# Kernel optimization log

Hardware: AMD Instinct MI355X
Metric: run time of the kernel (lower is better)

The kernel has to match this reference:

```python
import jax, jax.numpy as jnp
import numpy as np
from math import factorial

LMAX = 2
C_DIM = 128
N = 50000
# (l1, l2, l_out) 'uuu' (channel-wise, no weights) instructions, as in the module ([:3])
INSTR = [(2, 2, 0), (1, 2, 1), (1, 1, 2)]


def _f(n):
    return float(factorial(int(n)))


def _su2_cg(j1, m1, j2, m2, j3, m3):
    # Clebsch-Gordan <j1 m1 j2 m2 | j3 m3> (Racah formula), complex SU(2) basis
    if m3 != m1 + m2:
        return 0.0
    vmin = int(max(-j1 + j2 + m3, -j1 + m1, 0))
    vmax = int(min(j2 + j3 + m1, j3 - j1 + j2, j3 + m3))
    pref = ((2 * j3 + 1) * _f(j3 + j1 - j2) * _f(j3 - j1 + j2) * _f(j1 + j2 - j3) / _f(j1 + j2 + j3 + 1)
            * _f(j3 + m3) * _f(j3 - m3) / (_f(j1 - m1) * _f(j1 + m1) * _f(j2 - m2) * _f(j2 + m2))) ** 0.5
    s = 0.0
    for v in range(vmin, vmax + 1):
        s += (-1.0) ** (v + j2 + m2) / _f(v) * _f(j2 + j3 + m1 - v) * _f(j1 - m1 + v) / (
            _f(j3 - j1 + j2 - v) * _f(j3 + m3 - v) * _f(v + j1 - j2 - m3))
    return pref * s


def _q_real_to_complex(l):
    # e3nn change-of-basis from real to complex spherical harmonics
    q = np.zeros((2 * l + 1, 2 * l + 1), dtype=np.complex128)
    for m in range(-l, 0):
        q[l + m, l + abs(m)] = 1.0 / np.sqrt(2)
        q[l + m, l - abs(m)] = -1j / np.sqrt(2)
    q[l, l] = 1.0
    for m in range(1, l + 1):
        q[l + m, l + abs(m)] = (-1) ** m / np.sqrt(2)
        q[l + m, l - abs(m)] = 1j * (-1) ** m / np.sqrt(2)
    return (-1j) ** l * q


def wigner_3j(l1, l2, l3):
    # real-basis Wigner 3j, unit Frobenius norm (e3nn convention)
    Csu2 = np.zeros((2 * l1 + 1, 2 * l2 + 1, 2 * l3 + 1), dtype=np.complex128)
    for i, m1 in enumerate(range(-l1, l1 + 1)):
        for k, m2 in enumerate(range(-l2, l2 + 1)):
            for n, m3 in enumerate(range(-l3, l3 + 1)):
                Csu2[i, k, n] = _su2_cg(l1, m1, l2, m2, l3, m3)
    Q1, Q2, Q3 = _q_real_to_complex(l1), _q_real_to_complex(l2), _q_real_to_complex(l3)
    C = np.einsum('ij,kl,mn,ikn->jlm', Q1, Q2, np.conj(Q3.T), Csu2)
    assert np.abs(C.imag).max() < 1e-7
    C = C.real
    return (C / np.linalg.norm(C)).astype(np.float32)


W3J = {(l1, l2, lo): jnp.asarray(wigner_3j(l1, l2, lo)) for (l1, l2, lo) in INSTR}


def so3_linear(x, W, b):
    # per-degree block-diagonal linear; x: [N, (LMAX+1)^2, Cin], W: [LMAX+1, Cout, Cin], b: [Cout] (l=0 only)
    outs = []
    for l in range(LMAX + 1):
        y = jnp.einsum('nmc,dc->nmd', x[:, l * l:(l + 1) * (l + 1), :], W[l])
        if l == 0:
            y = y + b
        outs.append(y)
    return jnp.concatenate(outs, axis=1)


def tensor_product_uuu(x1, x2):
    # sparse CG tensor product, channel-shared ('uuu'), no path weights
    out = jnp.zeros_like(x1)
    for (l1, l2, lo) in INSTR:
        w3j = W3J[(l1, l2, lo)]
        alpha = float((2 * lo + 1) ** 0.5)  # component normalization
        blk = alpha * jnp.einsum('ijk,nic,njc->nkc', w3j,
                                 x1[:, l1 * l1:(l1 + 1) ** 2, :],
                                 x2[:, l2 * l2:(l2 + 1) ** 2, :])
        out = out.at[:, lo * lo:(lo + 1) ** 2, :].add(blk)
    return out


def setup_inputs() -> dict:
    key = jax.random.key(0)
    ks = jax.random.split(key, 7)
    scale = 1.0 / np.sqrt(C_DIM)
    m_dim = (LMAX + 1) ** 2  # 9
    return {
        'irreps_x': jax.random.normal(ks[0], (N, m_dim, C_DIM), jnp.float32),
        'W_left': jax.random.normal(ks[1], (LMAX + 1, C_DIM, C_DIM), jnp.float32) * scale,
        'b_left': jax.random.normal(ks[2], (C_DIM,), jnp.float32) * scale,
        'W_right': jax.random.normal(ks[3], (LMAX + 1, C_DIM, C_DIM), jnp.float32) * scale,
        'b_right': jax.random.normal(ks[4], (C_DIM,), jnp.float32) * scale,
        'W_final': jax.random.normal(ks[5], (LMAX + 1, C_DIM, C_DIM), jnp.float32) * scale,
        'b_final': jax.random.normal(ks[6], (C_DIM,), jnp.float32) * scale,
    }


def reference(irreps_x, W_left, b_left, W_right, b_right, W_final, b_final):
    xl = so3_linear(irreps_x, W_left, b_left)
    xr = so3_linear(irreps_x, W_right, b_right)
    out = tensor_product_uuu(xl, xr)
    return so3_linear(out, W_final, b_final)  # [N, 9, C]
```

## Files before the change

kernel.cpp:

```cpp
#include <hip/hip_runtime.h>
#include <cmath>
#include <complex>

typedef unsigned short u16;
typedef unsigned int u32;
typedef __bf16 bf16x8 __attribute__((ext_vector_type(8)));
typedef __bf16 bf16x2 __attribute__((ext_vector_type(2)));
typedef float f32x4 __attribute__((ext_vector_type(4)));
typedef float f32x2 __attribute__((ext_vector_type(2)));

#define CD 128
#define TILE_N 8
#define XS 136
#define LS 132

#define SMEM_TOTAL (72 * XS + 64 * LS + 64 * LS)

struct TPW { float w220[25]; float w121[45]; float w112[45]; };

__device__ __forceinline__ u32 pk2(float a, float b) {
  bf16x2 h;
  h.x = (__bf16)a;
  h.y = (__bf16)b;
  return __builtin_bit_cast(u32, h);
}
__device__ __forceinline__ f32x2 unpk(u32 v) {
  f32x2 r;
  r.x = __uint_as_float(v << 16);
  r.y = __uint_as_float(v & 0xffff0000u);
  return r;
}

__global__ void cvt_weights_kernel(const float* __restrict__ Wl,
                                   const float* __restrict__ Wr,
                                   const float* __restrict__ Wf,
                                   u16* __restrict__ ws) {
  int idx = (blockIdx.x * 256 + threadIdx.x) * 8;
  const float* src; int off;
  if (idx < 49152)      { src = Wl; off = idx; }
  else if (idx < 98304) { src = Wr; off = idx - 49152; }
  else                  { src = Wf; off = idx - 98304; }
  float4 a = *(const float4*)(src + off);
  float4 b = *(const float4*)(src + off + 4);
  uint4 v;
  v.x = pk2(a.x, a.y);
  v.y = pk2(a.z, a.w);
  v.z = pk2(b.x, b.y);
  v.w = pk2(b.z, b.w);
  *(uint4*)(ws + idx) = v;
}

__global__ __launch_bounds__(256, 3)
void fused_kernel(const float* __restrict__ x, const u16* __restrict__ ws,
                  const float* __restrict__ bfin, float* __restrict__ out,
                  int N, TPW tw) {
  __shared__ __align__(16) u16 smem[SMEM_TOTAL];
  u16* bufX = smem;
  u16* sTP  = smem;
  u16* sL   = smem + 72 * XS;
  u16* sR   = smem + 72 * XS + 64 * LS;

  const int tid  = threadIdx.x;
  const int n0   = blockIdx.x * TILE_N;
  const int w    = tid >> 6;
  const int lane = tid & 63;
  const int q    = lane >> 4;
  const int lr   = lane & 15;

  const int mat = w >> 1;
  const int wl  = w & 1;
  u16* dstA = mat ? sR : sL;
  const u16* wsA = ws + mat * 3 * 16384;

  uint4 bfa[2][2][4];
#pragma unroll
  for (int ci = 0; ci < 2; ++ci) {
    int dcol = (wl * 4 + ci) * 16 + lr;
#pragma unroll
    for (int kk = 0; kk < 4; ++kk) {
      bfa[ci][0][kk] = *(const uint4*)(wsA + 16384     + dcol * CD + kk * 32 + q * 8);
      bfa[ci][1][kk] = *(const uint4*)(wsA + 2 * 16384 + dcol * CD + kk * 32 + q * 8);
    }
  }
  const int dc0 = w * 16 + lr;
  const int dc1 = dc0 + 64;
  float bias0 = bfin[dc0];
  float bias1 = bfin[dc1];

#pragma unroll
  for (int it = 0; it < 4; ++it) {
    int e = (it * 256 + tid) * 8;
    int r = e >> 7;
    int c = e & 127;
    int n = n0 + (r & 7);
    if (n >= N) n = N - 1;
    int grow = (n * 9 + 1 + (r >> 3)) * CD + c;
    float4 a = *(const float4*)(x + grow);
    float4 b = *(const float4*)(x + grow + 4);
    uint4 v;
    v.x = pk2(a.x, a.y);
    v.y = pk2(a.z, a.w);
    v.z = pk2(b.x, b.y);
    v.w = pk2(b.z, b.w);
    *(uint4*)(bufX + r * XS + c) = v;
  }
  __syncthreads();

#pragma unroll
  for (int p = 0; p < 2; ++p) {
    if (p == 1) {
#pragma unroll
      for (int ci = 0; ci < 2; ++ci) {
        int dcol = (wl * 4 + 2 + ci) * 16 + lr;
#pragma unroll
        for (int kk = 0; kk < 4; ++kk) {
          bfa[ci][0][kk] = *(const uint4*)(wsA + 16384     + dcol * CD + kk * 32 + q * 8);
          bfa[ci][1][kk] = *(const uint4*)(wsA + 2 * 16384 + dcol * CD + kk * 32 + q * 8);
        }
      }
    }
#pragma unroll
    for (int rt = 0; rt < 5; ++rt) {
      const int l2f   = (rt >= 2) ? 1 : 0;
      const int rows  = l2f ? 40 : 24;
      const int gbase = l2f ? (rt - 2) * 16 : rt * 16;
      const int boff  = l2f ? 24 : 0;
      int ga = gbase + lr; if (ga > rows - 1) ga = rows - 1;
      const int arow = boff + ga;
      uint4 av[4];
#pragma unroll
      for (int kk = 0; kk < 4; ++kk)
        av[kk] = *(const uint4*)(bufX + arow * XS + kk * 32 + q * 8);
#pragma unroll
      for (int ci = 0; ci < 2; ++ci) {
        int dcol = (wl * 4 + 2 * p + ci) * 16 + lr;
        f32x4 acc = {0.f, 0.f, 0.f, 0.f};
#pragma unroll
        for (int kk = 0; kk < 4; ++kk) {
          acc = __builtin_amdgcn_mfma_f32_16x16x32_bf16(
              __builtin_bit_cast(bf16x8, av[kk]),
              __builtin_bit_cast(bf16x8, bfa[ci][l2f][kk]),
              acc, 0, 0, 0);
        }
        int g0 = gbase + q * 4;
        if (g0 < rows) {
          u32 p01 = pk2(acc[0], acc[1]);
          u32 p23 = pk2(acc[2], acc[3]);
          u16* d = dstA + (boff + g0) * LS + dcol;
          d[0]      = (u16)p01;
          d[LS]     = (u16)(p01 >> 16);
          d[2 * LS] = (u16)p23;
          d[3 * LS] = (u16)(p23 >> 16);
        }
      }
    }
  }
  __syncthreads();

#pragma unroll
  for (int iter = 0; iter < 2; ++iter) {
    int id = iter * 256 + tid;
    int cb = (id & 63) * 2;
    int n  = id >> 6;
    const u16* pL = sL + n * LS + cb;
    const u16* pR = sR + n * LS + cb;
    f32x2 xl1[3], xr1[3], xl2[5], xr2[5];
#pragma unroll
    for (int i = 0; i < 3; ++i) {
      xl1[i] = unpk(*(const u32*)(pL + i * 8 * LS));
      xr1[i] = unpk(*(const u32*)(pR + i * 8 * LS));
    }
#pragma unroll
    for (int j = 0; j < 5; ++j) {
      xl2[j] = unpk(*(const u32*)(pL + (24 + j * 8) * LS));
      xr2[j] = unpk(*(const u32*)(pR + (24 + j * 8) * LS));
    }
    f32x2 o0 = {0.f, 0.f};
#pragma unroll
    for (int i = 0; i < 5; ++i) {
      f32x2 t = {0.f, 0.f};
#pragma unroll
      for (int j = 0; j < 5; ++j) t += tw.w220[i * 5 + j] * xr2[j];
      o0 += xl2[i] * t;
    }
    f32x2 o1[3] = {{0.f,0.f},{0.f,0.f},{0.f,0.f}};
#pragma unroll
    for (int i = 0; i < 3; ++i)
#pragma unroll
      for (int j = 0; j < 5; ++j) {
        f32x2 pr = xl1[i] * xr2[j];
#pragma unroll
        for (int k = 0; k < 3; ++k) o1[k] += tw.w121[(i * 5 + j) * 3 + k] * pr;
      }
    f32x2 o2[5] = {{0.f,0.f},{0.f,0.f},{0.f,0.f},{0.f,0.f},{0.f,0.f}};
#pragma unroll
    for (int i = 0; i < 3; ++i)
#pragma unroll
      for (int j = 0; j < 3; ++j) {
        f32x2 pr = xl1[i] * xr1[j];
#pragma unroll
        for (int k = 0; k < 5; ++k) o2[k] += tw.w112[(i * 3 + j) * 5 + k] * pr;
      }
    u16* pT = sTP + n * XS + cb;
    *(u32*)(pT) = pk2(o0.x, o0.y);
#pragma unroll
    for (int k = 0; k < 3; ++k) *(u32*)(pT + (1 + k) * 8 * XS) = pk2(o1[k].x, o1[k].y);
#pragma unroll
    for (int k = 0; k < 5; ++k) *(u32*)(pT + (4 + k) * 8 * XS) = pk2(o2[k].x, o2[k].y);
  }

  const u16* wsf = ws + 6 * 16384;
  uint4 bc0[4], bc1[4];
#pragma unroll
  for (int kk = 0; kk < 4; ++kk) {
    bc0[kk] = *(const uint4*)(wsf + dc0 * CD + kk * 32 + q * 8);
    bc1[kk] = *(const uint4*)(wsf + dc1 * CD + kk * 32 + q * 8);
  }
  __syncthreads();

#pragma unroll
  for (int l = 0; l < 3; ++l) {
    if (l > 0) {
#pragma unroll
      for (int kk = 0; kk < 4; ++kk) {
        bc0[kk] = *(const uint4*)(wsf + l * 16384 + dc0 * CD + kk * 32 + q * 8);
        bc1[kk] = *(const uint4*)(wsf + l * 16384 + dc1 * CD + kk * 32 + q * 8);
      }
    }
    const int rows   = (l == 0) ? 8 : (l == 1 ? 24 : 40);
    const int soff   = (l == 0) ? 0 : (l == 1 ? 8 : 32);
    const int ntiles = (l == 0) ? 1 : (l == 1 ? 2 : 3);
#pragma unroll
    for (int t = 0; t < 3; ++t) {
      if (t >= ntiles) continue;
      int ga = t * 16 + lr; if (ga > rows - 1) ga = rows - 1;
      const int arow = soff + ga;
      uint4 av[4];
#pragma unroll
      for (int kk = 0; kk < 4; ++kk)
        av[kk] = *(const uint4*)(sTP + arow * XS + kk * 32 + q * 8);
      f32x4 a0 = {0.f, 0.f, 0.f, 0.f};
      f32x4 a1 = {0.f, 0.f, 0.f, 0.f};
#pragma unroll
      for (int kk = 0; kk < 4; ++kk) {
        a0 = __builtin_amdgcn_mfma_f32_16x16x32_bf16(
            __builtin_bit_cast(bf16x8, av[kk]),
            __builtin_bit_cast(bf16x8, bc0[kk]), a0, 0, 0, 0);
        a1 = __builtin_amdgcn_mfma_f32_16x16x32_bf16(
            __builtin_bit_cast(bf16x8, av[kk]),
            __builtin_bit_cast(bf16x8, bc1[kk]), a1, 0, 0, 0);
      }
#pragma unroll
      for (int reg = 0; reg < 4; ++reg) {
        int gg = t * 16 + q * 4 + reg;
        if (gg < rows) {
          int m = l * l + (gg >> 3);
          int n = n0 + (gg & 7);
          if (n < N) {
            float v0 = a0[reg], v1 = a1[reg];
            if (l == 0) { v0 += bias0; v1 += bias1; }
            out[(n * 9 + m) * CD + dc0] = v0;
            out[(n * 9 + m) * CD + dc1] = v1;
          }
        }
      }
    }
  }
}

typedef std::complex<double> cd;

static double factd(int n) { double r = 1.0; for (int i = 2; i <= n; ++i) r *= i; return r; }

static double su2_cg(int j1, int m1, int j2, int m2, int j3, int m3) {
  if (m3 != m1 + m2) return 0.0;
  int vmin = -j1 + j2 + m3; if (-j1 + m1 > vmin) vmin = -j1 + m1; if (0 > vmin) vmin = 0;
  int vmax = j2 + j3 + m1; if (j3 - j1 + j2 < vmax) vmax = j3 - j1 + j2; if (j3 + m3 < vmax) vmax = j3 + m3;
  double pref = std::sqrt((2.0 * j3 + 1.0) * factd(j3 + j1 - j2) * factd(j3 - j1 + j2)
                          * factd(j1 + j2 - j3) / factd(j1 + j2 + j3 + 1)
                          * factd(j3 + m3) * factd(j3 - m3)
                          / (factd(j1 - m1) * factd(j1 + m1) * factd(j2 - m2) * factd(j2 + m2)));
  double s = 0.0;
  for (int v = vmin; v <= vmax; ++v) {
    double sgn = ((v + j2 + m2) & 1) ? -1.0 : 1.0;
    s += sgn / factd(v) * factd(j2 + j3 + m1 - v) * factd(j1 - m1 + v)
         / (factd(j3 - j1 + j2 - v) * factd(j3 + m3 - v) * factd(v + j1 - j2 - m3));
  }
  return pref * s;
}

static void qmat(int l, cd q[5][5]) {
  for (int a = 0; a < 5; ++a) for (int b = 0; b < 5; ++b) q[a][b] = 0.0;
  const double is2 = 1.0 / std::sqrt(2.0);
  for (int m = -l; m < 0; ++m) {
    q[l + m][l - m] = is2;
    q[l + m][l + m] = cd(0.0, -is2);
  }
  q[l][l] = 1.0;
  for (int m = 1; m <= l; ++m) {
    double s = (m & 1) ? -1.0 : 1.0;
    q[l + m][l + m] = s * is2;
    q[l + m][l - m] = cd(0.0, s * is2);
  }
  cd f(1.0, 0.0);
  for (int i = 0; i < l; ++i) f *= cd(0.0, -1.0);
  for (int a = 0; a < 5; ++a) for (int b = 0; b < 5; ++b) q[a][b] *= f;
}

static void wigner3j(int l1, int l2, int l3, double* C) {
  int d1 = 2 * l1 + 1, d2 = 2 * l2 + 1, d3 = 2 * l3 + 1;
  cd Q1[5][5], Q2[5][5], Q3[5][5];
  qmat(l1, Q1); qmat(l2, Q2); qmat(l3, Q3);
  cd Csu2[5][5][5];
  for (int i = 0; i < d1; ++i)
    for (int k = 0; k < d2; ++k)
      for (int n = 0; n < d3; ++n)
        Csu2[i][k][n] = su2_cg(l1, i - l1, l2, k - l2, l3, n - l3);
  double norm = 0.0;
  for (int j = 0; j < d1; ++j)
    for (int lx = 0; lx < d2; ++lx)
      for (int m = 0; m < d3; ++m) {
        cd acc(0.0, 0.0);
        for (int i = 0; i < d1; ++i)
          for (int k = 0; k < d2; ++k)
            for (int n = 0; n < d3; ++n)
              acc += Q1[i][j] * Q2[k][lx] * std::conj(Q3[n][m]) * Csu2[i][k][n];
        C[(j * d2 + lx) * d3 + m] = acc.real();
        norm += acc.real() * acc.real();
      }
  norm = std::sqrt(norm);
  for (int t = 0; t < d1 * d2 * d3; ++t) C[t] /= norm;
}

extern "C" void kernel_launch(void* const* d_in, const int* in_sizes, int n_in,
                              void* d_out, int out_size, void* d_ws, size_t ws_size,
                              hipStream_t stream) {
  const float* x    = (const float*)d_in[0];
  const float* Wl   = (const float*)d_in[1];
  const float* Wr   = (const float*)d_in[3];
  const float* Wf   = (const float*)d_in[5];
  const float* bfin = (const float*)d_in[6];
  float* out = (float*)d_out;
  const int N = in_sizes[0] / (9 * CD);

  TPW tw;
  double c220[25], c121[45], c112[45];
  wigner3j(2, 2, 0, c220);
  wigner3j(1, 2, 1, c121);
  wigner3j(1, 1, 2, c112);
  const double a1 = std::sqrt(3.0), a2 = std::sqrt(5.0);
  for (int i = 0; i < 25; ++i) tw.w220[i] = (float)c220[i];
  for (int i = 0; i < 45; ++i) tw.w121[i] = (float)(a1 * c121[i]);
  for (int i = 0; i < 45; ++i) tw.w112[i] = (float)(a2 * c112[i]);

  u16* ws = (u16*)d_ws;
  cvt_weights_kernel<<<72, 256, 0, stream>>>(Wl, Wr, Wf, ws);
  int grid = (N + TILE_N - 1) / TILE_N;
  fused_kernel<<<grid, 256, 0, stream>>>(x, ws, bfin, out, N, tw);
}
```

Baseline: 489.5 us.

## Convert fused kernel to persistent grid-stride loop over node tiles

Launches a fixed grid of 768 blocks that loop over the 8-node tiles instead of one block per tile. The weight fragment loads are restructured so that each pass processes the l=1 and l=2 row tiles with two column blocks held in registers, reloading B fragments per phase. The intent is to cut block launch and scheduling overhead and to reuse per-block setup such as the bias loads. In exchange, weights are now reloaded every tile and there is an extra barrier per iteration, and the grid may be too small to hide latency.

```diff
diff --git a/kernel.cpp b/kernel.cpp
--- a/kernel.cpp
+++ b/kernel.cpp
@@ -13,6 +13,7 @@
 #define TILE_N 8
 #define XS 136
 #define LS 132
+#define GRID_BLOCKS 768
 
 #define SMEM_TOTAL (72 * XS + 64 * LS + 64 * LS)
 
@@ -29,6 +30,26 @@
   r.x = __uint_as_float(v << 16);
   r.y = __uint_as_float(v & 0xffff0000u);
   return r;
+}
+
+__device__ __forceinline__ void ldw4(uint4* dst, const u16* base) {
+#pragma unroll
+  for (int kk = 0; kk < 4; ++kk)
+    dst[kk] = *(const uint4*)(base + kk * 32);
+}
+
+__device__ __forceinline__ f32x4 mf(const uint4& a, const uint4& b, f32x4 c) {
+  return __builtin_amdgcn_mfma_f32_16x16x32_bf16(
+      __builtin_bit_cast(bf16x8, a), __builtin_bit_cast(bf16x8, b), c, 0, 0, 0);
+}
+
+__device__ __forceinline__ void stA(u16* d, const f32x4& a) {
+  u32 p01 = pk2(a[0], a[1]);
+  u32 p23 = pk2(a[2], a[3]);
+  d[0]      = (u16)p01;
+  d[LS]     = (u16)(p01 >> 16);
+  d[2 * LS] = (u16)p23;
+  d[3 * LS] = (u16)(p23 >> 16);
 }
 
 __global__ void cvt_weights_kernel(const float* __restrict__ Wl,
@@ -61,7 +82,6 @@
   u16* sR   = smem + 72 * XS + 64 * LS;
 
   const int tid  = threadIdx.x;
-  const int n0   = blockIdx.x * TILE_N;
   const int w    = tid >> 6;
   const int lane = tid & 63;
   const int q    = lane >> 4;
@@ -71,196 +91,188 @@
   const int wl  = w & 1;
   u16* dstA = mat ? sR : sL;
   const u16* wsA = ws + mat * 3 * 16384;
-
-  uint4 bfa[2][2][4];
-#pragma unroll
-  for (int ci = 0; ci < 2; ++ci) {
-    int dcol = (wl * 4 + ci) * 16 + lr;
-#pragma unroll
-    for (int kk = 0; kk < 4; ++kk) {
-      bfa[ci][0][kk] = *(const uint4*)(wsA + 16384     + dcol * CD + kk * 32 + q * 8);
-      bfa[ci][1][kk] = *(const uint4*)(wsA + 2 * 16384 + dcol * CD + kk * 32 + q * 8);
-    }
-  }
+  const u16* wsf = ws + 6 * 16384;
+
   const int dc0 = w * 16 + lr;
   const int dc1 = dc0 + 64;
-  float bias0 = bfin[dc0];
-  float bias1 = bfin[dc1];
-
-#pragma unroll
-  for (int it = 0; it < 4; ++it) {
-    int e = (it * 256 + tid) * 8;
-    int r = e >> 7;
-    int c = e & 127;
-    int n = n0 + (r & 7);
-    if (n >= N) n = N - 1;
-    int grow = (n * 9 + 1 + (r >> 3)) * CD + c;
-    float4 a = *(const float4*)(x + grow);
-    float4 b = *(const float4*)(x + grow + 4);
-    uint4 v;
-    v.x = pk2(a.x, a.y);
-    v.y = pk2(a.z, a.w);
-    v.z = pk2(b.x, b.y);
-    v.w = pk2(b.z, b.w);
-    *(uint4*)(bufX + r * XS + c) = v;
-  }
-  __syncthreads();
-
-#pragma unroll
-  for (int p = 0; p < 2; ++p) {
-    if (p == 1) {
-#pragma unroll
-      for (int ci = 0; ci < 2; ++ci) {
-        int dcol = (wl * 4 + 2 + ci) * 16 + lr;
+  const float bias0 = bfin[dc0];
+  const float bias1 = bfin[dc1];
+
+  const int ntiles = (N + TILE_N - 1) / TILE_N;
+
+  for (int tile = blockIdx.x; tile < ntiles; tile += gridDim.x) {
+    const int n0 = tile * TILE_N;
+
+    __syncthreads();
+
+#pragma unroll
+    for (int it = 0; it < 4; ++it) {
+      int e = (it * 256 + tid) * 8;
+      int r = e >> 7;
+      int c = e & 127;
+      int n = n0 + (r & 7);
+      if (n >= N) n = N - 1;
+      int grow = (n * 9 + 1 + (r >> 3)) * CD + c;
+      float4 a = *(const float4*)(x + grow);
+      float4 b = *(const float4*)(x + grow + 4);
+      uint4 v;
+      v.x = pk2(a.x, a.y);
+      v.y = pk2(a.z, a.w);
+      v.z = pk2(b.x, b.y);
+      v.w = pk2(b.z, b.w);
+      *(uint4*)(bufX + r * XS + c) = v;
+    }
+
+    uint4 bfA[4], bfB[4];
+    {
+      const int colA0 = wl * 64 + lr;
+      ldw4(bfA, wsA + 16384 + colA0 * CD + q * 8);
+      ldw4(bfB, wsA + 16384 + (colA0 + 16) * CD + q * 8);
+    }
+    __syncthreads();
+
+#pragma unroll
+    for (int p = 0; p < 2; ++p) {
+      const int colA = wl * 64 + p * 32 + lr;
+      const int colB = colA + 16;
+      if (p == 1) {
+        ldw4(bfA, wsA + 16384 + colA * CD + q * 8);
+        ldw4(bfB, wsA + 16384 + colB * CD + q * 8);
+      }
+#pragma unroll
+      for (int rt = 0; rt < 2; ++rt) {
+        const int gbase = rt * 16;
+        int ga = gbase + lr; if (ga > 23) ga = 23;
+        uint4 av[4];
+        ldw4(av, bufX + ga * XS + q * 8);
+        f32x4 accA = {0.f, 0.f, 0.f, 0.f};
+        f32x4 accB = {0.f, 0.f, 0.f, 0.f};
 #pragma unroll
         for (int kk = 0; kk < 4; ++kk) {
-          bfa[ci][0][kk] = *(const uint4*)(wsA + 16384     + dcol * CD + kk * 32 + q * 8);
-          bfa[ci][1][kk] = *(const uint4*)(wsA + 2 * 16384 + dcol * CD + kk * 32 + q * 8);
-        }
-      }
-    }
-#pragma unroll
-    for (int rt = 0; rt < 5; ++rt) {
-      const int l2f   = (rt >= 2) ? 1 : 0;
-      const int rows  = l2f ? 40 : 24;
-      const int gbase = l2f ? (rt - 2) * 16 : rt * 16;
-      const int boff  = l2f ? 24 : 0;
-      int ga = gbase + lr; if (ga > rows - 1) ga = rows - 1;
-      const int arow = boff + ga;
-      uint4 av[4];
-#pragma unroll
-      for (int kk = 0; kk < 4; ++kk)
-        av[kk] = *(const uint4*)(bufX + arow * XS + kk * 32 + q * 8);
-#pragma unroll
-      for (int ci = 0; ci < 2; ++ci) {
-        int dcol = (wl * 4 + 2 * p + ci) * 16 + lr;
-        f32x4 acc = {0.f, 0.f, 0.f, 0.f};
+          accA = mf(av[kk], bfA[kk], accA);
+          accB = mf(av[kk], bfB[kk], accB);
+        }
+        int g0 = gbase + q * 4;
+        if (g0 < 24) {
+          stA(dstA + g0 * LS + colA, accA);
+          stA(dstA + g0 * LS + colB, accB);
+        }
+      }
+      ldw4(bfA, wsA + 2 * 16384 + colA * CD + q * 8);
+      ldw4(bfB, wsA + 2 * 16384 + colB * CD + q * 8);
+#pragma unroll
+      for (int rt = 0; rt < 3; ++rt) {
+        const int gbase = rt * 16;
+        int ga = gbase + lr; if (ga > 39) ga = 39;
+        uint4 av[4];
+        ldw4(av, bufX + (24 + ga) * XS + q * 8);
+        f32x4 accA = {0.f, 0.f, 0.f, 0.f};
+        f32x4 accB = {0.f, 0.f, 0.f, 0.f};
 #pragma unroll
         for (int kk = 0; kk < 4; ++kk) {
-          acc = __builtin_amdgcn_mfma_f32_16x16x32_bf16(
-              __builtin_bit_cast(bf16x8, av[kk]),
-              __builtin_bit_cast(bf16x8, bfa[ci][l2f][kk]),
-              acc, 0, 0, 0);
+          accA = mf(av[kk], bfA[kk], accA);
+          accB = mf(av[kk], bfB[kk], accB);
         }
         int g0 = gbase + q * 4;
-        if (g0 < rows) {
-          u32 p01 = pk2(acc[0], acc[1]);
-          u32 p23 = pk2(acc[2], acc[3]);
-          u16* d = dstA + (boff + g0) * LS + dcol;
-          d[0]      = (u16)p01;
-          d[LS]     = (u16)(p01 >> 16);
-          d[2 * LS] = (u16)p23;
-          d[3 * LS] = (u16)(p23 >> 16);
-        }
-      }
-    }
-  }
-  __syncthreads();
-
-#pragma unroll
-  for (int iter = 0; iter < 2; ++iter) {
-    int id = iter * 256 + tid;
-    int cb = (id & 63) * 2;
-    int n  = id >> 6;
-    const u16* pL = sL + n * LS + cb;
-    const u16* pR = sR + n * LS + cb;
-    f32x2 xl1[3], xr1[3], xl2[5], xr2[5];
-#pragma unroll
-    for (int i = 0; i < 3; ++i) {
-      xl1[i] = unpk(*(const u32*)(pL + i * 8 * LS));
-      xr1[i] = unpk(*(const u32*)(pR + i * 8 * LS));
-    }
-#pragma unroll
-    for (int j = 0; j < 5; ++j) {
-      xl2[j] = unpk(*(const u32*)(pL + (24 + j * 8) * LS));
-      xr2[j] = unpk(*(const u32*)(pR + (24 + j * 8) * LS));
-    }
-    f32x2 o0 = {0.f, 0.f};
-#pragma unroll
-    for (int i = 0; i < 5; ++i) {
-      f32x2 t = {0.f, 0.f};
-#pragma unroll
-      for (int j = 0; j < 5; ++j) t += tw.w220[i * 5 + j] * xr2[j];
-      o0 += xl2[i] * t;
-    }
-    f32x2 o1[3] = {{0.f,0.f},{0.f,0.f},{0.f,0.f}};
-#pragma unroll
-    for (int i = 0; i < 3; ++i)
+        if (g0 < 40) {
+          stA(dstA + (24 + g0) * LS + colA, accA);
+          stA(dstA + (24 + g0) * LS + colB, accB);
+        }
+      }
+    }
+    __syncthreads();
+
+#pragma unroll
+    for (int iter = 0; iter < 2; ++iter) {
+      int id = iter * 256 + tid;
+      int cb = (id & 63) * 2;
+      int n  = id >> 6;
+      const u16* pL = sL + n * LS + cb;
+      const u16* pR = sR + n * LS + cb;
+      f32x2 xl1[3], xr1[3], xl2[5], xr2[5];
+#pragma unroll
+      for (int i = 0; i < 3; ++i) {
+        xl1[i] = unpk(*(const u32*)(pL + i * 8 * LS));
+        xr1[i] = unpk(*(const u32*)(pR + i * 8 * LS));
+      }
 #pragma unroll
       for (int j = 0; j < 5; ++j) {
-        f32x2 pr = xl1[i] * xr2[j];
-#pragma unroll
-        for (int k = 0; k < 3; ++k) o1[k] += tw.w121[(i * 5 + j) * 3 + k] * pr;
-      }
-    f32x2 o2[5] = {{0.f,0.f},{0.f,0.f},{0.f,0.f},{0.f,0.f},{0.f,0.f}};
-#pragma unroll
-    for (int i = 0; i < 3; ++i)
-#pragma unroll
-      for (int j = 0; j < 3; ++j) {
-        f32x2 pr = xl1[i] * xr1[j];
-#pragma unroll
-        for (int k = 0; k < 5; ++k) o2[k] += tw.w112[(i * 3 + j) * 5 + k] * pr;
-      }
-    u16* pT = sTP + n * XS + cb;
-    *(u32*)(pT) = pk2(o0.x, o0.y);
-#pragma unroll
-    for (int k = 0; k < 3; ++k) *(u32*)(pT + (1 + k) * 8 * XS) = pk2(o1[k].x, o1[k].y);
-#pragma unroll
-    for (int k = 0; k < 5; ++k) *(u32*)(pT + (4 + k) * 8 * XS) = pk2(o2[k].x, o2[k].y);
-  }
-
-  const u16* wsf = ws + 6 * 16384;
-  uint4 bc0[4], bc1[4];
-#pragma unroll
-  for (int kk = 0; kk < 4; ++kk) {
-    bc0[kk] = *(const uint4*)(wsf + dc0 * CD + kk * 32 + q * 8);
-    bc1[kk] = *(const uint4*)(wsf + dc1 * CD + kk * 32 + q * 8);
-  }
-  __syncthreads();
-
-#pragma unroll
-  for (int l = 0; l < 3; ++l) {
-    if (l > 0) {
-#pragma unroll
-      for (int kk = 0; kk < 4; ++kk) {
-        bc0[kk] = *(const uint4*)(wsf + l * 16384 + dc0 * CD + kk * 32 + q * 8);
-        bc1[kk] = *(const uint4*)(wsf + l * 16384 + dc1 * CD + kk * 32 + q * 8);
-      }
-    }
-    const int rows   = (l == 0) ? 8 : (l == 1 ? 24 : 40);
-    const int soff   = (l == 0) ? 0 : (l == 1 ? 8 : 32);
-    const int ntiles = (l == 0) ? 1 : (l == 1 ? 2 : 3);
-#pragma unroll
-    for (int t = 0; t < 3; ++t) {
-      if (t >= ntiles) continue;
-      int ga = t * 16 + lr; if (ga > rows - 1) ga = rows - 1;
-      const int arow = soff + ga;
-      uint4 av[4];
-#pragma unroll
-      for (int kk = 0; kk < 4; ++kk)
-        av[kk] = *(const uint4*)(sTP + arow * XS + kk * 32 + q * 8);
-      f32x4 a0 = {0.f, 0.f, 0.f, 0.f};
-      f32x4 a1 = {0.f, 0.f, 0.f, 0.f};
-#pragma unroll
-      for (int kk = 0; kk < 4; ++kk) {
-        a0 = __builtin_amdgcn_mfma_f32_16x16x32_bf16(
-            __builtin_bit_cast(bf16x8, av[kk]),
-            __builtin_bit_cast(bf16x8, bc0[kk]), a0, 0, 0, 0);
-        a1 = __builtin_amdgcn_mfma_f32_16x16x32_bf16(
-            __builtin_bit_cast(bf16x8, av[kk]),
-            __builtin_bit_cast(bf16x8, bc1[kk]), a1, 0, 0, 0);
-      }
-#pragma unroll
-      for (int reg = 0; reg < 4; ++reg) {
-        int gg = t * 16 + q * 4 + reg;
-        if (gg < rows) {
-          int m = l * l + (gg >> 3);
-          int n = n0 + (gg & 7);
-          if (n < N) {
-            float v0 = a0[reg], v1 = a1[reg];
-            if (l == 0) { v0 += bias0; v1 += bias1; }
-            out[(n * 9 + m) * CD + dc0] = v0;
-            out[(n * 9 + m) * CD + dc1] = v1;
+        xl2[j] = unpk(*(const u32*)(pL + (24 + j * 8) * LS));
+        xr2[j] = unpk(*(const u32*)(pR + (24 + j * 8) * LS));
+      }
+      f32x2 o0 = {0.f, 0.f};
+#pragma unroll
+      for (int i = 0; i < 5; ++i) {
+        f32x2 t = {0.f, 0.f};
+#pragma unroll
+        for (int j = 0; j < 5; ++j) t += tw.w220[i * 5 + j] * xr2[j];
+        o0 += xl2[i] * t;
+      }
+      f32x2 o1[3] = {{0.f,0.f},{0.f,0.f},{0.f,0.f}};
+#pragma unroll
+      for (int i = 0; i < 3; ++i)
+#pragma unroll
+        for (int j = 0; j < 5; ++j) {
+          f32x2 pr = xl1[i] * xr2[j];
+#pragma unroll
+          for (int k = 0; k < 3; ++k) o1[k] += tw.w121[(i * 5 + j) * 3 + k] * pr;
+        }
+      f32x2 o2[5] = {{0.f,0.f},{0.f,0.f},{0.f,0.f},{0.f,0.f},{0.f,0.f}};
+#pragma unroll
+      for (int i = 0; i < 3; ++i)
+#pragma unroll
+        for (int j = 0; j < 3; ++j) {
+          f32x2 pr = xl1[i] * xr1[j];
+#pragma unroll
+          for (int k = 0; k < 5; ++k) o2[k] += tw.w112[(i * 3 + j) * 5 + k] * pr;
+        }
+      u16* pT = sTP + n * XS + cb;
+      *(u32*)(pT) = pk2(o0.x, o0.y);
+#pragma unroll
+      for (int k = 0; k < 3; ++k) *(u32*)(pT + (1 + k) * 8 * XS) = pk2(o1[k].x, o1[k].y);
+#pragma unroll
+      for (int k = 0; k < 5; ++k) *(u32*)(pT + (4 + k) * 8 * XS) = pk2(o2[k].x, o2[k].y);
+    }
+
+    uint4 bc0[4], bc1[4];
+    ldw4(bc0, wsf + dc0 * CD + q * 8);
+    ldw4(bc1, wsf + dc1 * CD + q * 8);
+    __syncthreads();
+
+#pragma unroll
+    for (int l = 0; l < 3; ++l) {
+      if (l > 0) {
+        ldw4(bc0, wsf + l * 16384 + dc0 * CD + q * 8);
+        ldw4(bc1, wsf + l * 16384 + dc1 * CD + q * 8);
+      }
+      const int rows   = (l == 0) ? 8 : (l == 1 ? 24 : 40);
+      const int soff   = (l == 0) ? 0 : (l == 1 ? 8 : 32);
+      const int ntl    = (l == 0) ? 1 : (l == 1 ? 2 : 3);
+#pragma unroll
+      for (int t = 0; t < 3; ++t) {
+        if (t >= ntl) continue;
+        int ga = t * 16 + lr; if (ga > rows - 1) ga = rows - 1;
+        uint4 av[4];
+        ldw4(av, sTP + (soff + ga) * XS + q * 8);
+        f32x4 a0 = {0.f, 0.f, 0.f, 0.f};
+        f32x4 a1 = {0.f, 0.f, 0.f, 0.f};
+#pragma unroll
+        for (int kk = 0; kk < 4; ++kk) {
+          a0 = mf(av[kk], bc0[kk], a0);
+          a1 = mf(av[kk], bc1[kk], a1);
+        }
+#pragma unroll
+        for (int reg = 0; reg < 4; ++reg) {
+          int gg = t * 16 + q * 4 + reg;
+          if (gg < rows) {
+            int m = l * l + (gg >> 3);
+            int n = n0 + (gg & 7);
+            if (n < N) {
+              float v0 = a0[reg], v1 = a1[reg];
+              if (l == 0) { v0 += bias0; v1 += bias1; }
+              out[(n * 9 + m) * CD + dc0] = v0;
+              out[(n * 9 + m) * CD + dc1] = v1;
+            }
           }
         }
       }
@@ -355,6 +367,7 @@
 
   u16* ws = (u16*)d_ws;
   cvt_weights_kernel<<<72, 256, 0, stream>>>(Wl, Wr, Wf, ws);
-  int grid = (N + TILE_N - 1) / TILE_N;
+  int ntiles = (N + TILE_N - 1) / TILE_N;
+  int grid = ntiles < GRID_BLOCKS ? ntiles : GRID_BLOCKS;
   fused_kernel<<<grid, 256, 0, stream>>>(x, ws, bfin, out, N, tw);
 }
```

After: 577.3 us. +18.0%, slower.
